# Kernel tuning notes

Measured on AMD Instinct MI355X. Metric: run time of the kernel, lower is better.

The kernel has to match this reference:

```python
import jax, jax.numpy as jnp
import numpy as np

TILE = 16       # tile_size
R = 8           # search_radius
MAX_OFF = 8     # max initial offset magnitude used in setup
PAD = R + MAX_OFF  # padding so all gathers are in-bounds


def setup_inputs() -> dict:
    key = jax.random.key(0)
    k1, k2, k3 = jax.random.split(key, 3)
    B, C, H, W = 4, 3, 512, 512
    src = jax.random.normal(k1, (B, C, H, W), jnp.float32)
    dst = jax.random.normal(k2, (B, C, H, W), jnp.float32)
    offset = jax.random.randint(k3, (B, 2, H // TILE, W // TILE), 0, 9).astype(jnp.int32)
    return {"src": src, "dst": dst, "offset": offset}


def _gather_patches(img, rows, cols):
    # img: [C, Hp, Wp]; rows/cols: [nTH, nTW, K] -> [C, nTH, nTW, K, K]
    return img[:, rows[:, :, :, None], cols[:, :, None, :]]


def _tile_matching(src, dst, offset, tile=TILE, r=R, pad=PAD):
    B, C, H, W = src.shape
    nTH, nTW = H // tile, W // tile
    win = tile + 2 * r
    nD = 2 * r + 1

    dst_pad = jnp.pad(dst, ((0, 0), (0, 0), (pad, pad), (pad, pad)))
    off_y = offset[:, 0]  # [B, nTH, nTW]
    off_x = offset[:, 1]

    ti = (jnp.arange(nTH) * tile)  # tile origins (rows)
    tj = (jnp.arange(nTW) * tile)  # tile origins (cols)
    ar = jnp.arange(win)

    rows = ti[None, :, None, None] + off_y[..., None] + (pad - r) + ar
    cols = tj[None, None, :, None] + off_x[..., None] + (pad - r) + ar

    patches = jax.vmap(_gather_patches)(dst_pad, rows, cols)

    # Source tiles: [B, C, nTH, nTW, tile, tile]
    src_t = src.reshape(B, C, nTH, tile, nTW, tile).transpose(0, 1, 2, 4, 3, 5)

    def step(carry, d):
        best_c, best_i = carry
        dy, dx = d // nD, d % nD
        cand = jax.lax.dynamic_slice(
            patches, (0, 0, 0, 0, dy, dx), (B, C, nTH, nTW, tile, tile))
        cost = jnp.abs(cand - src_t).sum(axis=(1, 4, 5))  # SAD: [B, nTH, nTW]
        better = cost < best_c
        return (jnp.where(better, cost, best_c),
                jnp.where(better, d, best_i)), None

    init = (jnp.full((B, nTH, nTW), jnp.inf, src.dtype),
            jnp.zeros((B, nTH, nTW), jnp.int32))
    (best_c, best_i), _ = jax.lax.scan(step, init, jnp.arange(nD * nD, dtype=jnp.int32))

    dy = best_i // nD - r  # best displacement in [-r, r]
    dx = best_i % nD - r
    new_off = jnp.stack([off_y + dy, off_x + dx], axis=1)  # [B, 2, nTH, nTW]

    # Gather aligned dst tiles at refined offsets -> aligned image [B, C, H, W]
    art = jnp.arange(tile)
    rows2 = ti[None, :, None, None] + (off_y + dy)[..., None] + pad + art
    cols2 = tj[None, None, :, None] + (off_x + dx)[..., None] + pad + art
    aligned_t = jax.vmap(_gather_patches)(dst_pad, rows2, cols2)
    aligned = aligned_t.transpose(0, 1, 2, 4, 3, 5).reshape(B, C, H, W)
    return new_off, aligned


def reference(src, dst, offset):
    return _tile_matching(src, dst, offset)
```

## Files before the change

kernel.cpp:

```cpp
#include <hip/hip_runtime.h>

#define TILE 16
#define RR 8
#define ND 17
#define PW 544
#define PPAD 16
#define HH 512
#define WW 512
#define CC 3
#define BB 4
#define NTILES (BB * 1024)

typedef float f4a __attribute__((ext_vector_type(4), aligned(4)));
typedef unsigned long long u64;

__global__ __launch_bounds__(256) void pad_kernel(const float* __restrict__ dst,
                                                  float* __restrict__ P,
                                                  u64* __restrict__ keys) {
    const int gpr = PW / 4;
    const int gpi = PW * gpr;
    int idx = blockIdx.x * 256 + threadIdx.x;
    if (idx < NTILES) keys[idx] = ~0ULL;
    if (idx >= BB * CC * gpi) return;
    int bc  = idx / gpi;
    int rem = idx - bc * gpi;
    int y   = rem / gpr;
    int x   = (rem - y * gpr) * 4;
    float4 v = make_float4(0.f, 0.f, 0.f, 0.f);
    if (y >= PPAD && y < PPAD + HH && x >= PPAD && x < PPAD + WW)
        v = *(const float4*)(dst + ((size_t)bc * HH + (y - PPAD)) * WW + (x - PPAD));
    *(float4*)(P + ((size_t)bc * PW + y) * PW + x) = v;
}

template <int CTRL>
__device__ __forceinline__ float dpp_add(float x) {
    return x + __int_as_float(
        __builtin_amdgcn_update_dpp(0, __float_as_int(x), CTRL, 0xF, 0xF, true));
}
template <int MASK>
__device__ __forceinline__ float swz_add(float x) {
    int y = __builtin_amdgcn_ds_swizzle(__float_as_int(x), (MASK << 10) | 0x1F);
    return x + __int_as_float(y);
}

__global__ __launch_bounds__(576, 4) void sad_kernel(const float* __restrict__ src,
                                                     const float* __restrict__ P,
                                                     const int* __restrict__ offset,
                                                     u64* __restrict__ keys) {
    const int B = blockIdx.x;
    const int r = B & 7;
    const int q = B >> 3;
    const int tile = r * 512 + (q >> 1);
    const int dy = 8 * (q & 1) + (int)(threadIdx.x >> 6);

    const int b  = tile >> 10;
    const int th = (tile >> 5) & 31;
    const int tw = tile & 31;
    const int ti = th * TILE, tj = tw * TILE;
    const int oy = offset[(b * 2 + 0) * 1024 + th * 32 + tw];
    const int ox = offset[(b * 2 + 1) * 1024 + th * 32 + tw];

    const int l  = threadIdx.x & 63;
    const int h  = l & 1;
    const int jg = (l >> 1) & 1;
    const int i  = l >> 2;

    const int rowP = ti + oy + (PPAD - RR) + dy + i;
    const int colW = tj + ox + (PPAD - RR) + 8 * (h + jg);

    float W[CC][16];
    float S[CC][8];
    #pragma unroll
    for (int c = 0; c < CC; ++c) {
        const float* wp = P + ((size_t)((b * CC + c) * PW + rowP)) * PW + colW;
        f4a a0 = *(const f4a*)(wp + 0);
        f4a a1 = *(const f4a*)(wp + 4);
        f4a a2 = *(const f4a*)(wp + 8);
        f4a a3 = *(const f4a*)(wp + 12);
        W[c][0]=a0.x;  W[c][1]=a0.y;  W[c][2]=a0.z;  W[c][3]=a0.w;
        W[c][4]=a1.x;  W[c][5]=a1.y;  W[c][6]=a1.z;  W[c][7]=a1.w;
        W[c][8]=a2.x;  W[c][9]=a2.y;  W[c][10]=a2.z; W[c][11]=a2.w;
        W[c][12]=a3.x; W[c][13]=a3.y; W[c][14]=a3.z; W[c][15]=a3.w;
        const float* sp = src + ((size_t)((b * CC + c) * HH + ti + i)) * WW + tj + 8 * jg;
        f4a s0 = *(const f4a*)sp;
        f4a s1 = *(const f4a*)(sp + 4);
        S[c][0]=s0.x; S[c][1]=s0.y; S[c][2]=s0.z; S[c][3]=s0.w;
        S[c][4]=s1.x; S[c][5]=s1.y; S[c][6]=s1.z; S[c][7]=s1.w;
    }

    float acc[9];
    #pragma unroll
    for (int a = 0; a < 9; ++a) acc[a] = 0.f;
    #pragma unroll
    for (int c = 0; c < CC; ++c) {
        #pragma unroll
        for (int a = 0; a < 9; ++a) {
            float s0 = acc[a];
            #pragma unroll
            for (int jl = 0; jl < 8; ++jl)
                s0 += fabsf(W[c][a + jl] - S[c][jl]);
            acc[a] = s0;
        }
    }

    #pragma unroll
    for (int a = 0; a < 9; ++a) {
        float x = acc[a];
        x = dpp_add<0x4E>(x);
        x = swz_add<4>(x);
        x = swz_add<8>(x);
        x = swz_add<16>(x);
        x += __shfl_xor(x, 32);
        acc[a] = x;
    }

    float bc = h ? acc[1] : acc[0];
    int   ba = h;
    #pragma unroll
    for (int a = 1; a < 9; ++a)
        if (a > h && acc[a] < bc) { bc = acc[a]; ba = a; }
    const unsigned d = (unsigned)(dy * ND + 8 * h + ba);
    u64 key = ((u64)__float_as_uint(bc) << 32) | d;
    u64 ok  = __shfl_xor(key, 1);
    if (ok < key) key = ok;
    if (l == 0) atomicMin(keys + tile, key);
}

__global__ __launch_bounds__(256) void gather_kernel(const float* __restrict__ P,
                                                     const int* __restrict__ offset,
                                                     const u64* __restrict__ keys,
                                                     float* __restrict__ out) {
    const int tile = blockIdx.x * 4 + (int)(threadIdx.x >> 6);
    const int b  = tile >> 10;
    const int th = (tile >> 5) & 31;
    const int tw = tile & 31;
    const int ti = th * TILE, tj = tw * TILE;
    const int t  = threadIdx.x & 63;
    const int oy = offset[(b * 2 + 0) * 1024 + th * 32 + tw];
    const int ox = offset[(b * 2 + 1) * 1024 + th * 32 + tw];
    const int d  = (int)(keys[tile] & 0xFFFFFFFFu);
    const int bdy = d / ND;
    const int bdx = d - bdy * ND;

    if (t == 0) out[(b * 2 + 0) * 1024 + th * 32 + tw] = (float)(oy + bdy - RR);
    if (t == 1) out[(b * 2 + 1) * 1024 + th * 32 + tw] = (float)(ox + bdx - RR);

    float* aligned = out + BB * 2 * 1024;
    const int pr = ti + oy + bdy + (PPAD - RR);
    const int pc = tj + ox + bdx + (PPAD - RR);
    #pragma unroll
    for (int k = 0; k < 12; ++k) {
        int idx = t + 64 * k;
        int c  = idx >> 8;
        int ii = (idx >> 4) & 15;
        int jj = idx & 15;
        aligned[((size_t)((b * CC + c) * HH + ti + ii)) * WW + tj + jj] =
            P[((size_t)((b * CC + c) * PW + pr + ii)) * PW + pc + jj];
    }
}

extern "C" void kernel_launch(void* const* d_in, const int* in_sizes, int n_in,
                              void* d_out, int out_size, void* d_ws, size_t ws_size,
                              hipStream_t stream) {
    const float* src    = (const float*)d_in[0];
    const float* dst    = (const float*)d_in[1];
    const int*   offset = (const int*)d_in[2];
    float*       out    = (float*)d_out;

    float* P = (float*)d_ws;
    u64* keys = (u64*)(P + (size_t)BB * CC * PW * PW);

    const int pad_groups = BB * CC * PW * (PW / 4);
    pad_kernel<<<dim3(pad_groups / 256), 256, 0, stream>>>(dst, P, keys);
    sad_kernel<<<dim3(NTILES * 2), 576, 0, stream>>>(src, P, offset, keys);
    gather_kernel<<<dim3(NTILES / 4), 256, 0, stream>>>(P, offset, keys, out);
}
```

Measured before the change: 135.1 us.

## Fuse pad, SAD search and gather into one LDS-staged per-tile kernel

Replaces the three-kernel pipeline (global padded copy of dst, SAD kernel with global atomicMin keys, gather kernel) with a single kernel per tile. Each block stages the 32x32 search window (zero-filled at borders) and the source tile into LDS, each wave runs one or two dy rows of the SAD search, and the block reduces its keys in shared memory before writing the aligned tile straight from LDS. This removes the padded-buffer write and read, the atomics, and two launches. In exchange each block does more serial work, waves 0-7 take a second pass while wave 8 does not, and the border checks add branches to the load path.

```diff
diff --git a/kernel.cpp b/kernel.cpp
--- a/kernel.cpp
+++ b/kernel.cpp
@@ -3,34 +3,17 @@
 #define TILE 16
 #define RR 8
 #define ND 17
-#define PW 544
-#define PPAD 16
 #define HH 512
 #define WW 512
 #define CC 3
 #define BB 4
-#define NTILES (BB * 1024)
+#define WROWS 32
+#define WSTR 36
+#define SSTR 20
+#define BLK 576
 
 typedef float f4a __attribute__((ext_vector_type(4), aligned(4)));
 typedef unsigned long long u64;
-
-__global__ __launch_bounds__(256) void pad_kernel(const float* __restrict__ dst,
-                                                  float* __restrict__ P,
-                                                  u64* __restrict__ keys) {
-    const int gpr = PW / 4;
-    const int gpi = PW * gpr;
-    int idx = blockIdx.x * 256 + threadIdx.x;
-    if (idx < NTILES) keys[idx] = ~0ULL;
-    if (idx >= BB * CC * gpi) return;
-    int bc  = idx / gpi;
-    int rem = idx - bc * gpi;
-    int y   = rem / gpr;
-    int x   = (rem - y * gpr) * 4;
-    float4 v = make_float4(0.f, 0.f, 0.f, 0.f);
-    if (y >= PPAD && y < PPAD + HH && x >= PPAD && x < PPAD + WW)
-        v = *(const float4*)(dst + ((size_t)bc * HH + (y - PPAD)) * WW + (x - PPAD));
-    *(float4*)(P + ((size_t)bc * PW + y) * PW + x) = v;
-}
 
 template <int CTRL>
 __device__ __forceinline__ float dpp_add(float x) {
@@ -43,66 +26,29 @@
     return x + __int_as_float(y);
 }
 
-__global__ __launch_bounds__(576, 4) void sad_kernel(const float* __restrict__ src,
-                                                     const float* __restrict__ P,
-                                                     const int* __restrict__ offset,
-                                                     u64* __restrict__ keys) {
-    const int B = blockIdx.x;
-    const int r = B & 7;
-    const int q = B >> 3;
-    const int tile = r * 512 + (q >> 1);
-    const int dy = 8 * (q & 1) + (int)(threadIdx.x >> 6);
-
-    const int b  = tile >> 10;
-    const int th = (tile >> 5) & 31;
-    const int tw = tile & 31;
-    const int ti = th * TILE, tj = tw * TILE;
-    const int oy = offset[(b * 2 + 0) * 1024 + th * 32 + tw];
-    const int ox = offset[(b * 2 + 1) * 1024 + th * 32 + tw];
-
-    const int l  = threadIdx.x & 63;
-    const int h  = l & 1;
-    const int jg = (l >> 1) & 1;
-    const int i  = l >> 2;
-
-    const int rowP = ti + oy + (PPAD - RR) + dy + i;
-    const int colW = tj + ox + (PPAD - RR) + 8 * (h + jg);
-
-    float W[CC][16];
-    float S[CC][8];
-    #pragma unroll
-    for (int c = 0; c < CC; ++c) {
-        const float* wp = P + ((size_t)((b * CC + c) * PW + rowP)) * PW + colW;
-        f4a a0 = *(const f4a*)(wp + 0);
-        f4a a1 = *(const f4a*)(wp + 4);
-        f4a a2 = *(const f4a*)(wp + 8);
-        f4a a3 = *(const f4a*)(wp + 12);
-        W[c][0]=a0.x;  W[c][1]=a0.y;  W[c][2]=a0.z;  W[c][3]=a0.w;
-        W[c][4]=a1.x;  W[c][5]=a1.y;  W[c][6]=a1.z;  W[c][7]=a1.w;
-        W[c][8]=a2.x;  W[c][9]=a2.y;  W[c][10]=a2.z; W[c][11]=a2.w;
-        W[c][12]=a3.x; W[c][13]=a3.y; W[c][14]=a3.z; W[c][15]=a3.w;
-        const float* sp = src + ((size_t)((b * CC + c) * HH + ti + i)) * WW + tj + 8 * jg;
-        f4a s0 = *(const f4a*)sp;
-        f4a s1 = *(const f4a*)(sp + 4);
-        S[c][0]=s0.x; S[c][1]=s0.y; S[c][2]=s0.z; S[c][3]=s0.w;
-        S[c][4]=s1.x; S[c][5]=s1.y; S[c][6]=s1.z; S[c][7]=s1.w;
-    }
-
+__device__ __forceinline__ u64 sad_pass(const float* Wl, const float S[CC][8],
+                                        int dy, int i, int h, int jg) {
     float acc[9];
     #pragma unroll
     for (int a = 0; a < 9; ++a) acc[a] = 0.f;
     #pragma unroll
     for (int c = 0; c < CC; ++c) {
+        const int wb = c * (WROWS * WSTR) + (dy + i) * WSTR + 8 * (h + jg);
+        f4a a0 = *(const f4a*)&Wl[wb + 0];
+        f4a a1 = *(const f4a*)&Wl[wb + 4];
+        f4a a2 = *(const f4a*)&Wl[wb + 8];
+        f4a a3 = *(const f4a*)&Wl[wb + 12];
+        float W16[16] = { a0.x, a0.y, a0.z, a0.w, a1.x, a1.y, a1.z, a1.w,
+                          a2.x, a2.y, a2.z, a2.w, a3.x, a3.y, a3.z, a3.w };
         #pragma unroll
         for (int a = 0; a < 9; ++a) {
             float s0 = acc[a];
             #pragma unroll
             for (int jl = 0; jl < 8; ++jl)
-                s0 += fabsf(W[c][a + jl] - S[c][jl]);
+                s0 += fabsf(W16[a + jl] - S[c][jl]);
             acc[a] = s0;
         }
     }
-
     #pragma unroll
     for (int a = 0; a < 9; ++a) {
         float x = acc[a];
@@ -113,7 +59,6 @@
         x += __shfl_xor(x, 32);
         acc[a] = x;
     }
-
     float bc = h ? acc[1] : acc[0];
     int   ba = h;
     #pragma unroll
@@ -122,23 +67,93 @@
     const unsigned d = (unsigned)(dy * ND + 8 * h + ba);
     u64 key = ((u64)__float_as_uint(bc) << 32) | d;
     u64 ok  = __shfl_xor(key, 1);
-    if (ok < key) key = ok;
-    if (l == 0) atomicMin(keys + tile, key);
+    return ok < key ? ok : key;
 }
 
-__global__ __launch_bounds__(256) void gather_kernel(const float* __restrict__ P,
-                                                     const int* __restrict__ offset,
-                                                     const u64* __restrict__ keys,
-                                                     float* __restrict__ out) {
-    const int tile = blockIdx.x * 4 + (int)(threadIdx.x >> 6);
+__global__ __launch_bounds__(BLK, 6) void tile_kernel(const float* __restrict__ src,
+                                                      const float* __restrict__ dst,
+                                                      const int* __restrict__ offset,
+                                                      float* __restrict__ out) {
+    __shared__ float Wl[CC * WROWS * WSTR];
+    __shared__ float Sl[CC * TILE * SSTR];
+    __shared__ u64   keyL[9];
+
+    const int bid  = blockIdx.x;
+    const int tile = ((bid & 7) << 9) | (bid >> 3);
     const int b  = tile >> 10;
     const int th = (tile >> 5) & 31;
     const int tw = tile & 31;
     const int ti = th * TILE, tj = tw * TILE;
-    const int t  = threadIdx.x & 63;
     const int oy = offset[(b * 2 + 0) * 1024 + th * 32 + tw];
     const int ox = offset[(b * 2 + 1) * 1024 + th * 32 + tw];
-    const int d  = (int)(keys[tile] & 0xFFFFFFFFu);
+    const int t  = threadIdx.x;
+
+    const int gy0 = ti + oy - RR;
+    const int gx0 = tj + ox - RR;
+    for (int k = t; k < CC * WROWS * 8; k += BLK) {
+        int c   = k >> 8;
+        int rem = k & 255;
+        int row = rem >> 3;
+        int cc  = (rem & 7) << 2;
+        int gy = gy0 + row;
+        int gx = gx0 + cc;
+        float4 v = make_float4(0.f, 0.f, 0.f, 0.f);
+        if ((unsigned)gy < HH) {
+            const float* p = dst + ((size_t)(b * CC + c) * HH + gy) * WW;
+            if ((unsigned)gx <= WW - 4) {
+                f4a u = *(const f4a*)(p + gx);
+                v = make_float4(u.x, u.y, u.z, u.w);
+            } else {
+                float* ve = (float*)&v;
+                #pragma unroll
+                for (int e = 0; e < 4; ++e) {
+                    int g = gx + e;
+                    if ((unsigned)g < WW) ve[e] = p[g];
+                }
+            }
+        }
+        *(f4a*)&Wl[c * (WROWS * WSTR) + row * WSTR + cc] = *(f4a*)&v;
+    }
+    if (t >= 192 && t < 384) {
+        int k   = t - 192;
+        int c   = k >> 6;
+        int rem = k & 63;
+        int row = rem >> 2;
+        int cc  = (rem & 3) << 2;
+        f4a v = *(const f4a*)(src + ((size_t)(b * CC + c) * HH + ti + row) * WW + tj + cc);
+        *(f4a*)&Sl[c * (TILE * SSTR) + row * SSTR + cc] = v;
+    }
+    __syncthreads();
+
+    const int wv = t >> 6;
+    const int l  = t & 63;
+    const int h  = l & 1;
+    const int jg = (l >> 1) & 1;
+    const int i  = l >> 2;
+
+    float S[CC][8];
+    #pragma unroll
+    for (int c = 0; c < CC; ++c) {
+        const int sb = c * (TILE * SSTR) + i * SSTR + 8 * jg;
+        f4a s0 = *(const f4a*)&Sl[sb];
+        f4a s1 = *(const f4a*)&Sl[sb + 4];
+        S[c][0]=s0.x; S[c][1]=s0.y; S[c][2]=s0.z; S[c][3]=s0.w;
+        S[c][4]=s1.x; S[c][5]=s1.y; S[c][6]=s1.z; S[c][7]=s1.w;
+    }
+
+    u64 bestkey = sad_pass(Wl, S, wv, i, h, jg);
+    const int dy2 = 9 + wv;
+    if (dy2 < ND) {
+        u64 k2 = sad_pass(Wl, S, dy2, i, h, jg);
+        if (k2 < bestkey) bestkey = k2;
+    }
+    if (l == 0) keyL[wv] = bestkey;
+    __syncthreads();
+
+    u64 wk = keyL[0];
+    #pragma unroll
+    for (int w = 1; w < 9; ++w) { u64 kw = keyL[w]; if (kw < wk) wk = kw; }
+    const int d   = (int)(wk & 0xFFFFFFFFu);
     const int bdy = d / ND;
     const int bdx = d - bdy * ND;
 
@@ -146,16 +161,12 @@
     if (t == 1) out[(b * 2 + 1) * 1024 + th * 32 + tw] = (float)(ox + bdx - RR);
 
     float* aligned = out + BB * 2 * 1024;
-    const int pr = ti + oy + bdy + (PPAD - RR);
-    const int pc = tj + ox + bdx + (PPAD - RR);
-    #pragma unroll
-    for (int k = 0; k < 12; ++k) {
-        int idx = t + 64 * k;
-        int c  = idx >> 8;
-        int ii = (idx >> 4) & 15;
-        int jj = idx & 15;
-        aligned[((size_t)((b * CC + c) * HH + ti + ii)) * WW + tj + jj] =
-            P[((size_t)((b * CC + c) * PW + pr + ii)) * PW + pc + jj];
+    for (int e = t; e < CC * TILE * TILE; e += BLK) {
+        int c  = e >> 8;
+        int ii = (e >> 4) & 15;
+        int jj = e & 15;
+        aligned[((size_t)(b * CC + c) * HH + ti + ii) * WW + tj + jj] =
+            Wl[c * (WROWS * WSTR) + (bdy + ii) * WSTR + bdx + jj];
     }
 }
 
@@ -166,12 +177,5 @@
     const float* dst    = (const float*)d_in[1];
     const int*   offset = (const int*)d_in[2];
     float*       out    = (float*)d_out;
-
-    float* P = (float*)d_ws;
-    u64* keys = (u64*)(P + (size_t)BB * CC * PW * PW);
-
-    const int pad_groups = BB * CC * PW * (PW / 4);
-    pad_kernel<<<dim3(pad_groups / 256), 256, 0, stream>>>(dst, P, keys);
-    sad_kernel<<<dim3(NTILES * 2), 576, 0, stream>>>(src, P, offset, keys);
-    gather_kernel<<<dim3(NTILES / 4), 256, 0, stream>>>(P, offset, keys, out);
+    tile_kernel<<<dim3(BB * 1024), BLK, 0, stream>>>(src, dst, offset, out);
 }
```

After: 130.3 us. -3.5%, faster.
